# Kernel tuning notes

Measured on AMD Instinct MI355X. Metric: run time of the kernel, lower is better.

Reference implementation:

```python
import jax, jax.numpy as jnp
import numpy as np

B, S, HID = 4, 1024, 1024
NH, HD = 16, 64  # num_heads, head_size
LEFT, RIGHT = 64, 8
NUM_POS = LEFT + RIGHT + 1  # 73


def setup_inputs() -> dict:
    key = jax.random.key(0)
    ks = jax.random.split(key, 11)
    s = 0.02
    return {
        "hidden_states": jax.random.normal(ks[0], (B, S, HID), jnp.float32),
        "Wq": jax.random.normal(ks[1], (HID, HID), jnp.float32) * s,
        "bq": jax.random.normal(ks[2], (HID,), jnp.float32) * s,
        "Wk": jax.random.normal(ks[3], (HID, HID), jnp.float32) * s,
        "bk": jax.random.normal(ks[4], (HID,), jnp.float32) * s,
        "Wv": jax.random.normal(ks[5], (HID, HID), jnp.float32) * s,
        "bv": jax.random.normal(ks[6], (HID,), jnp.float32) * s,
        "Wo": jax.random.normal(ks[7], (HID, HID), jnp.float32) * s,
        "bo": jax.random.normal(ks[8], (HID,), jnp.float32) * s,
        "dist_emb": jax.random.normal(ks[9], (NUM_POS, HD), jnp.float32) * s,
    }


def reference(hidden_states, Wq, bq, Wk, bk, Wv, bv, Wo, bo, dist_emb):
    inv_sqrt_d = 1.0 / np.sqrt(HD).astype(np.float32)
    # projections; nn.Linear: x @ W.T + b
    q = (hidden_states @ Wq.T + bq).reshape(B, S, NH, HD).transpose(0, 2, 1, 3)  # bhld
    k = (hidden_states @ Wk.T + bk).reshape(B, S, NH, HD).transpose(0, 2, 1, 3)
    v = (hidden_states @ Wv.T + bv).reshape(B, S, NH, HD).transpose(0, 2, 1, 3)

    scores = jnp.einsum("bhld,bhrd->bhlr", q, k) * inv_sqrt_d

    # relative_key bias
    pos_l = jnp.arange(S)[:, None]
    pos_r = jnp.arange(S)[None, :]
    dist = jnp.clip(pos_r - pos_l, -LEFT, RIGHT) + LEFT  # [S,S] in [0, NUM_POS)
    pos_emb = dist_emb[dist]  # [S,S,HD]
    rel = jnp.einsum("bhld,lrd->bhlr", q, pos_emb) * inv_sqrt_d
    scores = scores + rel

    probs = jax.nn.softmax(scores, axis=-1)  # dropout p=0 (eval)
    ctx = jnp.einsum("bhlr,bhrd->bhld", probs, v)
    ctx = ctx.transpose(0, 2, 1, 3).reshape(B, S, HID)
    out = ctx @ Wo.T + bo
    return (out, probs)
```

## Files before the change

kernel.cpp:

```cpp
#include <hip/hip_runtime.h>


using short8 = __attribute__((ext_vector_type(8))) short;
using f32x4  = __attribute__((ext_vector_type(4))) float;
using fl4    = __attribute__((ext_vector_type(4))) float;
using u16x4  = __attribute__((ext_vector_type(4))) unsigned short;

#define MFMA16(a, b, c) __builtin_amdgcn_mfma_f32_16x16x32_bf16((a), (b), (c), 0, 0, 0)

#define SCL2E 0.18033688011112042f

__device__ __forceinline__ float bf2f(unsigned short u) {
  union { unsigned int i; float f; } c;
  c.i = ((unsigned int)u) << 16;
  return c.f;
}
__device__ __forceinline__ unsigned short f2bf(float f) {
  union { float f; unsigned int i; } c;
  c.f = f;
  unsigned int x = c.i;
  return (unsigned short)((x + 0x7fffu + ((x >> 16) & 1u)) >> 16);
}
__device__ __forceinline__ float u2f(unsigned u) {
  union { unsigned i; float f; } c;
  c.i = u;
  return c.f;
}

__device__ __forceinline__ void gload_lds16(const void* g, void* l) {
  __builtin_amdgcn_global_load_lds(
      (const __attribute__((address_space(1))) void*)g,
      (__attribute__((address_space(3))) void*)l, 16, 0, 0);
}

__global__ void cvt_f32_bf16(const float* __restrict__ in,
                             unsigned short* __restrict__ out, int n4) {
  int i = blockIdx.x * blockDim.x + threadIdx.x;
  int stride = gridDim.x * blockDim.x;
  for (; i < n4; i += stride) {
    fl4 v = ((const fl4*)in)[i];
    u16x4 o;
    o[0] = f2bf(v[0]); o[1] = f2bf(v[1]); o[2] = f2bf(v[2]); o[3] = f2bf(v[3]);
    ((u16x4*)out)[i] = o;
  }
}

__global__ void cvt_w4d(const float* __restrict__ w0, const float* __restrict__ w1,
                        const float* __restrict__ w2, const float* __restrict__ w3,
                        const float* __restrict__ de,
                        unsigned short* __restrict__ o0, unsigned short* __restrict__ o1,
                        unsigned short* __restrict__ o2, unsigned short* __restrict__ o3,
                        unsigned short* __restrict__ od) {
  if (blockIdx.x == 1024) {
    for (int i = threadIdx.x; i < 80 * 64; i += 256)
      od[i] = (i < 73 * 64) ? f2bf(de[i]) : (unsigned short)0;
    return;
  }
  const int which = blockIdx.x >> 8;
  const float* in = which == 0 ? w0 : which == 1 ? w1 : which == 2 ? w2 : w3;
  unsigned short* out = which == 0 ? o0 : which == 1 ? o1 : which == 2 ? o2 : o3;
  int i = (blockIdx.x & 255) * 256 + threadIdx.x;
#pragma unroll
  for (int it = 0; it < 4; ++it, i += 65536) {
    fl4 v = ((const fl4*)in)[i];
    u16x4 o;
    o[0] = f2bf(v[0]); o[1] = f2bf(v[1]); o[2] = f2bf(v[2]); o[3] = f2bf(v[3]);
    ((u16x4*)out)[i] = o;
  }
}

__global__ __launch_bounds__(256)
void gemm_qkv3(const unsigned short* __restrict__ X,
               const unsigned short* __restrict__ Bq,
               const unsigned short* __restrict__ Bk,
               const unsigned short* __restrict__ Bv,
               const float* __restrict__ biq, const float* __restrict__ bik,
               const float* __restrict__ biv,
               unsigned short* __restrict__ Cq, unsigned short* __restrict__ Ck,
               unsigned short* __restrict__ Cv) {
  __shared__ unsigned short lA[128 * 32];
  __shared__ unsigned short lB[128 * 32];
  const int i = blockIdx.x;
  const int wgid = (i & 7) * 96 + (i >> 3);
  const int r = wgid >> 8;
  const int id = wgid & 255;
  int bm, bn;
  const unsigned short *Aa, *Bb;
  if (r == 2) {
    bm = (id >> 5) * 128; bn = (id & 31) * 128;
    Aa = Bv; Bb = X;
  } else {
    bm = (id >> 3) * 128; bn = (id & 7) * 128;
    Aa = X; Bb = (r == 0) ? Bq : Bk;
  }
  const float* bias = (r == 0) ? biq : (r == 1) ? bik : biv;

  const int tid = threadIdx.x;
  const int wave = tid >> 6, lane = tid & 63;
  const int wm = wave >> 1, wn = wave & 1;

  f32x4 acc[4][4];
#pragma unroll
  for (int m = 0; m < 4; ++m)
#pragma unroll
    for (int n = 0; n < 4; ++n) acc[m][n] = (f32x4){0.f, 0.f, 0.f, 0.f};

  const int t0 = tid, t1 = tid + 256;
  const int ar0 = t0 >> 2, ak0 = (t0 & 3) * 8;
  const int ar1 = t1 >> 2, ak1 = (t1 & 3) * 8;
  const unsigned short* Ab = Aa + (size_t)bm * 1024;
  const unsigned short* Bbb = Bb + (size_t)bn * 1024;
  const int fr = lane & 15, fk = (lane >> 4) * 8;

  for (int kt = 0; kt < 1024; kt += 32) {
    gload_lds16(Ab + (size_t)ar0 * 1024 + kt + ak0, (void*)&lA[(wave * 64) * 8]);
    gload_lds16(Ab + (size_t)ar1 * 1024 + kt + ak1, (void*)&lA[2048 + (wave * 64) * 8]);
    gload_lds16(Bbb + (size_t)ar0 * 1024 + kt + ak0, (void*)&lB[(wave * 64) * 8]);
    gload_lds16(Bbb + (size_t)ar1 * 1024 + kt + ak1, (void*)&lB[2048 + (wave * 64) * 8]);
    __syncthreads();
    short8 af[4], bf[4];
#pragma unroll
    for (int m = 0; m < 4; ++m)
      af[m] = *(const short8*)&lA[(wm * 64 + m * 16 + fr) * 32 + fk];
#pragma unroll
    for (int n = 0; n < 4; ++n)
      bf[n] = *(const short8*)&lB[(wn * 64 + n * 16 + fr) * 32 + fk];
#pragma unroll
    for (int m = 0; m < 4; ++m)
#pragma unroll
      for (int n = 0; n < 4; ++n) acc[m][n] = MFMA16(af[m], bf[n], acc[m][n]);
    __syncthreads();
  }

  const int cr = (lane >> 4) * 4, cc = lane & 15;
#pragma unroll
  for (int m = 0; m < 4; ++m)
#pragma unroll
    for (int n = 0; n < 4; ++n) {
      const int col = bn + wn * 64 + n * 16 + cc;
#pragma unroll
      for (int g = 0; g < 4; ++g) {
        const int row = bm + wm * 64 + m * 16 + cr + g;
        if (r == 2) {
          const float v = acc[m][n][g] + bias[row];
          const int head = row >> 6, d = row & 63;
          const int b2 = col >> 10, sl = col & 1023, kk = sl & 31;
          size_t idx = ((size_t)((b2 << 4) + head) << 16) +
                       (size_t)(((sl >> 5) * 4 + (d >> 4)) * 512) +
                       (d & 15) * 32 + ((kk >> 3) * 8) + (kk & 7);
          Cv[idx] = f2bf(v);
        } else {
          const float v = acc[m][n][g] + bias[col];
          const int head = col >> 6, d = col & 63;
          const int b2 = row >> 10, sl = row & 1023;
          const int dc = d >> 3;
          const size_t hb = (size_t)((b2 << 4) + head) << 16;
          if (r == 0) {
            size_t idx = hb +
                         (size_t)((((sl >> 4) * 2 + (dc >> 2)) * 16 + (sl & 15)) * 32) +
                         (dc & 3) * 8 + (d & 7);
            Cq[idx] = f2bf(v);
          } else {
            const int kt2 = sl >> 5;
            const int p = ((sl >> 3) & 3) * 4 + (sl & 3);
            const int half = (sl >> 2) & 1;
            size_t idx = hb +
                         (size_t)((((kt2 * 2 + half) * 2 + (dc >> 2)) * 512)) +
                         p * 32 + (dc & 3) * 8 + (d & 7);
            Ck[idx] = f2bf(v);
          }
        }
      }
    }
}

__global__ __launch_bounds__(256)
void gemm_nt_f32(const unsigned short* __restrict__ A,
                 const unsigned short* __restrict__ B,
                 const float* __restrict__ bias, float* __restrict__ Cp) {
  __shared__ unsigned short lA[128 * 32];
  __shared__ unsigned short lB[128 * 32];
  const int tid = threadIdx.x;
  const int wave = tid >> 6, lane = tid & 63;
  const int wm = wave >> 1, wn = wave & 1;
  const int bm = blockIdx.x * 128, bn = blockIdx.y * 128;

  f32x4 acc[4][4];
#pragma unroll
  for (int m = 0; m < 4; ++m)
#pragma unroll
    for (int n = 0; n < 4; ++n) acc[m][n] = (f32x4){0.f, 0.f, 0.f, 0.f};

  const int t0 = tid, t1 = tid + 256;
  const int ar0 = t0 >> 2, ak0 = (t0 & 3) * 8;
  const int ar1 = t1 >> 2, ak1 = (t1 & 3) * 8;
  const unsigned short* Ab = A + (size_t)bm * 1024;
  const unsigned short* Bb = B + (size_t)bn * 1024;
  const int fr = lane & 15, fk = (lane >> 4) * 8;

  for (int kt = 0; kt < 1024; kt += 32) {
    gload_lds16(Ab + (size_t)ar0 * 1024 + kt + ak0, (void*)&lA[(wave * 64) * 8]);
    gload_lds16(Ab + (size_t)ar1 * 1024 + kt + ak1, (void*)&lA[2048 + (wave * 64) * 8]);
    gload_lds16(Bb + (size_t)ar0 * 1024 + kt + ak0, (void*)&lB[(wave * 64) * 8]);
    gload_lds16(Bb + (size_t)ar1 * 1024 + kt + ak1, (void*)&lB[2048 + (wave * 64) * 8]);
    __syncthreads();
    short8 af[4], bf[4];
#pragma unroll
    for (int m = 0; m < 4; ++m)
      af[m] = *(const short8*)&lA[(wm * 64 + m * 16 + fr) * 32 + fk];
#pragma unroll
    for (int n = 0; n < 4; ++n)
      bf[n] = *(const short8*)&lB[(wn * 64 + n * 16 + fr) * 32 + fk];
#pragma unroll
    for (int m = 0; m < 4; ++m)
#pragma unroll
      for (int n = 0; n < 4; ++n) acc[m][n] = MFMA16(af[m], bf[n], acc[m][n]);
    __syncthreads();
  }

  const int cr = (lane >> 4) * 4, cc = lane & 15;
#pragma unroll
  for (int m = 0; m < 4; ++m)
#pragma unroll
    for (int n = 0; n < 4; ++n) {
      const int col = bn + wn * 64 + n * 16 + cc;
#pragma unroll
      for (int g = 0; g < 4; ++g) {
        const int row = bm + wm * 64 + m * 16 + cr + g;
        Cp[(size_t)row * 1024 + col] = acc[m][n][g] + bias[col];
      }
    }
}

__global__ __launch_bounds__(256, 2)
void attn_kernel(const unsigned short* __restrict__ q,
                 const unsigned short* __restrict__ k,
                 const unsigned short* __restrict__ vt,
                 const unsigned short* __restrict__ demb_bf,
                 float* __restrict__ probs,
                 unsigned short* __restrict__ ctx) {
  const int i = blockIdx.x;
  const int x = i & 7, s = i >> 3;
  const int bh = ((s >> 5) << 3) + x;
  const int qseg = s & 31;
  const int hd = bh & 15, b = bh >> 4;
  const int tid = threadIdx.x, w = tid >> 6, lane = tid & 63;
  const int lq = lane & 15, Qr = lane >> 4;
  const int qA = qseg * 32, qB = qA + 16;

  __shared__ unsigned short qdc[32][78];
  __shared__ float reds[4][32];
  __shared__ float red[4][4][32][16];

  const size_t hb = (size_t)((b << 4) + hd) << 16;
  const int lo16 = lq * 32 + Qr * 8;

  const unsigned short* qh = q + hb + (size_t)(qseg * 4) * 512;
  short8 bqA0 = *(const short8*)(qh + lo16);
  short8 bqA1 = *(const short8*)(qh + 512 + lo16);
  short8 bqB0 = *(const short8*)(qh + 1024 + lo16);
  short8 bqB1 = *(const short8*)(qh + 1536 + lo16);

  for (int pgq = w; pgq < 10; pgq += 4) {
    const int qblk = pgq >= 5;
    const int pg = qblk ? pgq - 5 : pgq;
    const unsigned short* dp = demb_bf + (size_t)(pg * 16 + lq) * 64 + Qr * 8;
    short8 a0 = *(const short8*)dp;
    short8 a1 = *(const short8*)(dp + 32);
    f32x4 c = (f32x4){0.f, 0.f, 0.f, 0.f};
    c = MFMA16(a0, qblk ? bqB0 : bqA0, c);
    c = MFMA16(a1, qblk ? bqB1 : bqA1, c);
#pragma unroll
    for (int g = 0; g < 4; ++g) {
      const int p = pg * 16 + Qr * 4 + g;
      if (p < 73) qdc[qblk * 16 + lq][p] = f2bf(c[g] * SCL2E);
    }
  }
  __syncthreads();

  const float qd0A = bf2f(qdc[lq][0]),       qd72A = bf2f(qdc[lq][72]);
  const float qd0B = bf2f(qdc[16 + lq][0]),  qd72B = bf2f(qdc[16 + lq][72]);

  float ssumA = 0.f, ssumB = 0.f;
  unsigned pafA[8][4], pafB[8][4];

  const unsigned short* kh = k + hb + (size_t)(w * 8) * 2048 + lo16;
  const unsigned short* vh = vt + hb + (size_t)(w * 8) * 2048 + lo16;

#pragma unroll
  for (int t = 0; t < 8; ++t) {
    const unsigned short* kp = kh + t * 2048;
    short8 ae0 = *(const short8*)kp;
    short8 ae1 = *(const short8*)(kp + 512);
    short8 ao0 = *(const short8*)(kp + 1024);
    short8 ao1 = *(const short8*)(kp + 1536);

    f32x4 seA = (f32x4){0.f, 0.f, 0.f, 0.f}, soA = seA, seB = seA, soB = seA;
    seA = MFMA16(ae0, bqA0, seA); seA = MFMA16(ae1, bqA1, seA);
    soA = MFMA16(ao0, bqA0, soA); soA = MFMA16(ao1, bqA1, soA);
    seB = MFMA16(ae0, bqB0, seB); seB = MFMA16(ae1, bqB1, seB);
    soB = MFMA16(ao0, bqB0, soB); soB = MFMA16(ao1, bqB1, soB);

    const int tglob = w * 8 + t;
    {
      float pe[4], po[4];
      if (tglob * 32 + 31 < qA - 64) {
#pragma unroll
        for (int g = 0; g < 4; ++g) {
          pe[g] = exp2f(fmaf(seA[g], SCL2E, qd0A));
          po[g] = exp2f(fmaf(soA[g], SCL2E, qd0A));
        }
      } else if (tglob * 32 > qA + 23) {
#pragma unroll
        for (int g = 0; g < 4; ++g) {
          pe[g] = exp2f(fmaf(seA[g], SCL2E, qd72A));
          po[g] = exp2f(fmaf(soA[g], SCL2E, qd72A));
        }
      } else {
        const int c0 = tglob * 32 + Qr * 8 - (qA + lq);
#pragma unroll
        for (int g = 0; g < 4; ++g) {
          int d0 = c0 + g;     d0 = d0 < -64 ? -64 : (d0 > 8 ? 8 : d0);
          int d1 = c0 + 4 + g; d1 = d1 < -64 ? -64 : (d1 > 8 ? 8 : d1);
          pe[g] = exp2f(fmaf(seA[g], SCL2E, bf2f(qdc[lq][d0 + 64])));
          po[g] = exp2f(fmaf(soA[g], SCL2E, bf2f(qdc[lq][d1 + 64])));
        }
      }
#pragma unroll
      for (int g = 0; g < 4; ++g) ssumA += pe[g] + po[g];
      asm("v_cvt_pk_bf16_f32 %0, %1, %2" : "=v"(pafA[t][0]) : "v"(pe[0]), "v"(pe[1]));
      asm("v_cvt_pk_bf16_f32 %0, %1, %2" : "=v"(pafA[t][1]) : "v"(pe[2]), "v"(pe[3]));
      asm("v_cvt_pk_bf16_f32 %0, %1, %2" : "=v"(pafA[t][2]) : "v"(po[0]), "v"(po[1]));
      asm("v_cvt_pk_bf16_f32 %0, %1, %2" : "=v"(pafA[t][3]) : "v"(po[2]), "v"(po[3]));
    }
    {
      float pe[4], po[4];
      if (tglob * 32 + 31 < qB - 64) {
#pragma unroll
        for (int g = 0; g < 4; ++g) {
          pe[g] = exp2f(fmaf(seB[g], SCL2E, qd0B));
          po[g] = exp2f(fmaf(soB[g], SCL2E, qd0B));
        }
      } else if (tglob * 32 > qB + 23) {
#pragma unroll
        for (int g = 0; g < 4; ++g) {
          pe[g] = exp2f(fmaf(seB[g], SCL2E, qd72B));
          po[g] = exp2f(fmaf(soB[g], SCL2E, qd72B));
        }
      } else {
        const int c0 = tglob * 32 + Qr * 8 - (qB + lq);
#pragma unroll
        for (int g = 0; g < 4; ++g) {
          int d0 = c0 + g;     d0 = d0 < -64 ? -64 : (d0 > 8 ? 8 : d0);
          int d1 = c0 + 4 + g; d1 = d1 < -64 ? -64 : (d1 > 8 ? 8 : d1);
          pe[g] = exp2f(fmaf(seB[g], SCL2E, bf2f(qdc[16 + lq][d0 + 64])));
          po[g] = exp2f(fmaf(soB[g], SCL2E, bf2f(qdc[16 + lq][d1 + 64])));
        }
      }
#pragma unroll
      for (int g = 0; g < 4; ++g) ssumB += pe[g] + po[g];
      asm("v_cvt_pk_bf16_f32 %0, %1, %2" : "=v"(pafB[t][0]) : "v"(pe[0]), "v"(pe[1]));
      asm("v_cvt_pk_bf16_f32 %0, %1, %2" : "=v"(pafB[t][1]) : "v"(pe[2]), "v"(pe[3]));
      asm("v_cvt_pk_bf16_f32 %0, %1, %2" : "=v"(pafB[t][2]) : "v"(po[0]), "v"(po[1]));
      asm("v_cvt_pk_bf16_f32 %0, %1, %2" : "=v"(pafB[t][3]) : "v"(po[2]), "v"(po[3]));
    }
  }
  ssumA += __shfl_xor(ssumA, 16, 64);
  ssumA += __shfl_xor(ssumA, 32, 64);
  ssumB += __shfl_xor(ssumB, 16, 64);
  ssumB += __shfl_xor(ssumB, 32, 64);
  if (lane < 16) {
    reds[w][lane] = ssumA;
    reds[w][16 + lane] = ssumB;
  }
  __syncthreads();

  const float invA =
      1.0f / (reds[0][lq] + reds[1][lq] + reds[2][lq] + reds[3][lq]);
  const float invB = 1.0f / (reds[0][16 + lq] + reds[1][16 + lq] +
                             reds[2][16 + lq] + reds[3][16 + lq]);
  float* prowA = probs + ((size_t)bh * 1024 + qA + lq) * 1024 + w * 256 + Qr * 8;
  float* prowB = prowA + (size_t)16 * 1024;

  f32x4 oA0 = (f32x4){0.f, 0.f, 0.f, 0.f}, oA1 = oA0, oA2 = oA0, oA3 = oA0;
  f32x4 oB0 = oA0, oB1 = oA0, oB2 = oA0, oB3 = oA0;
#pragma unroll
  for (int t = 0; t < 8; ++t) {
    const unsigned short* vp = vh + t * 2048;
    short8 v0 = *(const short8*)vp;
    short8 v1 = *(const short8*)(vp + 512);
    short8 v2 = *(const short8*)(vp + 1024);
    short8 v3 = *(const short8*)(vp + 1536);

    union { unsigned u[4]; short8 s8v; } ua, ub;
    ua.u[0] = pafA[t][0]; ua.u[1] = pafA[t][1];
    ua.u[2] = pafA[t][2]; ua.u[3] = pafA[t][3];
    ub.u[0] = pafB[t][0]; ub.u[1] = pafB[t][1];
    ub.u[2] = pafB[t][2]; ub.u[3] = pafB[t][3];
    const short8 pa = ua.s8v, pb = ub.s8v;
    oA0 = MFMA16(pa, v0, oA0);
    oA1 = MFMA16(pa, v1, oA1);
    oA2 = MFMA16(pa, v2, oA2);
    oA3 = MFMA16(pa, v3, oA3);
    oB0 = MFMA16(pb, v0, oB0);
    oB1 = MFMA16(pb, v1, oB1);
    oB2 = MFMA16(pb, v2, oB2);
    oB3 = MFMA16(pb, v3, oB3);

    f32x4 p0, p1;
    p0[0] = u2f(pafA[t][0] << 16) * invA;
    p0[1] = u2f(pafA[t][0] & 0xffff0000u) * invA;
    p0[2] = u2f(pafA[t][1] << 16) * invA;
    p0[3] = u2f(pafA[t][1] & 0xffff0000u) * invA;
    p1[0] = u2f(pafA[t][2] << 16) * invA;
    p1[1] = u2f(pafA[t][2] & 0xffff0000u) * invA;
    p1[2] = u2f(pafA[t][3] << 16) * invA;
    p1[3] = u2f(pafA[t][3] & 0xffff0000u) * invA;
    *(f32x4*)&prowA[t * 32] = p0;
    *(f32x4*)&prowA[t * 32 + 4] = p1;
    f32x4 q0, q1;
    q0[0] = u2f(pafB[t][0] << 16) * invB;
    q0[1] = u2f(pafB[t][0] & 0xffff0000u) * invB;
    q0[2] = u2f(pafB[t][1] << 16) * invB;
    q0[3] = u2f(pafB[t][1] & 0xffff0000u) * invB;
    q1[0] = u2f(pafB[t][2] << 16) * invB;
    q1[1] = u2f(pafB[t][2] & 0xffff0000u) * invB;
    q1[2] = u2f(pafB[t][3] << 16) * invB;
    q1[3] = u2f(pafB[t][3] & 0xffff0000u) * invB;
    *(f32x4*)&prowB[t * 32] = q0;
    *(f32x4*)&prowB[t * 32 + 4] = q1;
  }

#pragma unroll
  for (int g = 0; g < 4; ++g) {
    red[w][0][Qr * 4 + g][lq] = oA0[g];
    red[w][1][Qr * 4 + g][lq] = oA1[g];
    red[w][2][Qr * 4 + g][lq] = oA2[g];
    red[w][3][Qr * 4 + g][lq] = oA3[g];
    red[w][0][16 + Qr * 4 + g][lq] = oB0[g];
    red[w][1][16 + Qr * 4 + g][lq] = oB1[g];
    red[w][2][16 + Qr * 4 + g][lq] = oB2[g];
    red[w][3][16 + Qr * 4 + g][lq] = oB3[g];
  }
  __syncthreads();

  {
    const int qrow = tid >> 3;
    const int d0 = (tid & 7) * 8;
    const float invq = 1.0f / (reds[0][qrow] + reds[1][qrow] +
                               reds[2][qrow] + reds[3][qrow]);
    u16x4 cv0, cv1;
#pragma unroll
    for (int j = 0; j < 8; ++j) {
      const int d = d0 + j;
      const int db = d >> 4, dd = d & 15;
      float sum = red[0][db][qrow][dd] + red[1][db][qrow][dd] +
                  red[2][db][qrow][dd] + red[3][db][qrow][dd];
      if (j < 4) cv0[j] = f2bf(sum * invq);
      else       cv1[j - 4] = f2bf(sum * invq);
    }
    unsigned short* cb =
        ctx + ((size_t)(b * 1024 + qA + qrow)) * 1024 + hd * 64 + d0;
    *(u16x4*)cb = cv0;
    *(u16x4*)(cb + 4) = cv1;
  }
}

extern "C" void kernel_launch(void* const* d_in, const int* in_sizes, int n_in,
                              void* d_out, int out_size, void* d_ws, size_t ws_size,
                              hipStream_t stream) {
  const float* hs = (const float*)d_in[0];
  const float* Wq = (const float*)d_in[1];
  const float* bq = (const float*)d_in[2];
  const float* Wk = (const float*)d_in[3];
  const float* bk = (const float*)d_in[4];
  const float* Wv = (const float*)d_in[5];
  const float* bv = (const float*)d_in[6];
  const float* Wo = (const float*)d_in[7];
  const float* bo = (const float*)d_in[8];
  const float* de = (const float*)d_in[9];

  float* out = (float*)d_out;
  float* probs = out + (size_t)4 * 1024 * 1024;

  char* ws = (char*)d_ws;
  unsigned short* Xb  = (unsigned short*)(ws);
  unsigned short* Wqb = (unsigned short*)(ws + ((size_t)8 << 20));
  unsigned short* Wkb = (unsigned short*)(ws + ((size_t)10 << 20));
  unsigned short* Wvb = (unsigned short*)(ws + ((size_t)12 << 20));
  unsigned short* Wob = (unsigned short*)(ws + ((size_t)14 << 20));
  unsigned short* Qb  = (unsigned short*)(ws + ((size_t)16 << 20));
  unsigned short* Kb  = (unsigned short*)(ws + ((size_t)24 << 20));
  unsigned short* Vt  = (unsigned short*)(ws + ((size_t)32 << 20));
  unsigned short* Db  = (unsigned short*)(ws + ((size_t)40 << 20));
  unsigned short* Cx  = Xb;

  cvt_f32_bf16<<<dim3(1024), dim3(256), 0, stream>>>(hs, Xb, (4 * 1024 * 1024) / 4);
  cvt_w4d<<<dim3(1025), dim3(256), 0, stream>>>(Wq, Wk, Wv, Wo, de,
                                                Wqb, Wkb, Wvb, Wob, Db);

  gemm_qkv3<<<dim3(768), dim3(256), 0, stream>>>(Xb, Wqb, Wkb, Wvb, bq, bk, bv,
                                                 Qb, Kb, Vt);

  attn_kernel<<<dim3(2048), dim3(256), 0, stream>>>(Qb, Kb, Vt, Db, probs, Cx);

  gemm_nt_f32<<<dim3(32, 8), dim3(256), 0, stream>>>(Cx, Wob, bo, out);
}
```

Measured before the change: 173.6 us.

## Process two 32-query tiles per attention block, overlapping second QK with first PV

New measurement: 200.4 us. +15.4%, slower.

```diff
diff --git a/kernel.cpp b/kernel.cpp
--- a/kernel.cpp
+++ b/kernel.cpp
@@ -241,52 +241,110 @@
                  unsigned short* __restrict__ ctx) {
   const int i = blockIdx.x;
   const int x = i & 7, s = i >> 3;
-  const int bh = ((s >> 5) << 3) + x;
-  const int qseg = s & 31;
+  const int bh = ((s >> 4) << 3) + x;
+  const int j = s & 15;
   const int hd = bh & 15, b = bh >> 4;
   const int tid = threadIdx.x, w = tid >> 6, lane = tid & 63;
   const int lq = lane & 15, Qr = lane >> 4;
-  const int qA = qseg * 32, qB = qA + 16;
-
-  __shared__ unsigned short qdc[32][78];
-  __shared__ float reds[4][32];
+  const int qA1 = j * 64, qB1 = qA1 + 16, qA2 = qA1 + 32, qB2 = qA1 + 48;
+
+  __shared__ unsigned short qdc[2][32][78];
+  __shared__ float reds[2][4][32];
   __shared__ float red[4][4][32][16];
 
   const size_t hb = (size_t)((b << 4) + hd) << 16;
   const int lo16 = lq * 32 + Qr * 8;
 
-  const unsigned short* qh = q + hb + (size_t)(qseg * 4) * 512;
-  short8 bqA0 = *(const short8*)(qh + lo16);
-  short8 bqA1 = *(const short8*)(qh + 512 + lo16);
-  short8 bqB0 = *(const short8*)(qh + 1024 + lo16);
-  short8 bqB1 = *(const short8*)(qh + 1536 + lo16);
-
-  for (int pgq = w; pgq < 10; pgq += 4) {
-    const int qblk = pgq >= 5;
-    const int pg = qblk ? pgq - 5 : pgq;
+  const unsigned short* qh1 = q + hb + (size_t)(j * 8) * 512;
+  const unsigned short* qh2 = qh1 + 2048;
+  short8 q1A0 = *(const short8*)(qh1 + lo16);
+  short8 q1A1 = *(const short8*)(qh1 + 512 + lo16);
+  short8 q1B0 = *(const short8*)(qh1 + 1024 + lo16);
+  short8 q1B1 = *(const short8*)(qh1 + 1536 + lo16);
+  short8 q2A0 = *(const short8*)(qh2 + lo16);
+  short8 q2A1 = *(const short8*)(qh2 + 512 + lo16);
+  short8 q2B0 = *(const short8*)(qh2 + 1024 + lo16);
+  short8 q2B1 = *(const short8*)(qh2 + 1536 + lo16);
+
+  for (int pgq = w; pgq < 20; pgq += 4) {
+    const int u = pgq >= 10;
+    const int pp = pgq - u * 10;
+    const int qblk = pp >= 5;
+    const int pg = pp - qblk * 5;
     const unsigned short* dp = demb_bf + (size_t)(pg * 16 + lq) * 64 + Qr * 8;
     short8 a0 = *(const short8*)dp;
     short8 a1 = *(const short8*)(dp + 32);
+    short8 f0 = u ? (qblk ? q2B0 : q2A0) : (qblk ? q1B0 : q1A0);
+    short8 f1 = u ? (qblk ? q2B1 : q2A1) : (qblk ? q1B1 : q1A1);
     f32x4 c = (f32x4){0.f, 0.f, 0.f, 0.f};
-    c = MFMA16(a0, qblk ? bqB0 : bqA0, c);
-    c = MFMA16(a1, qblk ? bqB1 : bqA1, c);
+    c = MFMA16(a0, f0, c);
+    c = MFMA16(a1, f1, c);
 #pragma unroll
     for (int g = 0; g < 4; ++g) {
       const int p = pg * 16 + Qr * 4 + g;
-      if (p < 73) qdc[qblk * 16 + lq][p] = f2bf(c[g] * SCL2E);
+      if (p < 73) qdc[u][qblk * 16 + lq][p] = f2bf(c[g] * SCL2E);
     }
   }
   __syncthreads();
 
-  const float qd0A = bf2f(qdc[lq][0]),       qd72A = bf2f(qdc[lq][72]);
-  const float qd0B = bf2f(qdc[16 + lq][0]),  qd72B = bf2f(qdc[16 + lq][72]);
-
-  float ssumA = 0.f, ssumB = 0.f;
-  unsigned pafA[8][4], pafB[8][4];
+  const float qd0A1 = bf2f(qdc[0][lq][0]),      qd72A1 = bf2f(qdc[0][lq][72]);
+  const float qd0B1 = bf2f(qdc[0][16 + lq][0]), qd72B1 = bf2f(qdc[0][16 + lq][72]);
+  const float qd0A2 = bf2f(qdc[1][lq][0]),      qd72A2 = bf2f(qdc[1][lq][72]);
+  const float qd0B2 = bf2f(qdc[1][16 + lq][0]), qd72B2 = bf2f(qdc[1][16 + lq][72]);
 
   const unsigned short* kh = k + hb + (size_t)(w * 8) * 2048 + lo16;
   const unsigned short* vh = vt + hb + (size_t)(w * 8) * 2048 + lo16;
 
+#define QKEXP(se, so, qAx, qd0x, qd72x, UU, LQOFF, paf, ssum, tglob)          \
+  {                                                                           \
+    float pe[4], po[4];                                                       \
+    if ((tglob)*32 + 31 < (qAx)-64) {                                         \
+      _Pragma("unroll") for (int g = 0; g < 4; ++g) {                         \
+        pe[g] = exp2f(fmaf(se[g], SCL2E, qd0x));                              \
+        po[g] = exp2f(fmaf(so[g], SCL2E, qd0x));                              \
+      }                                                                       \
+    } else if ((tglob)*32 > (qAx) + 23) {                                     \
+      _Pragma("unroll") for (int g = 0; g < 4; ++g) {                         \
+        pe[g] = exp2f(fmaf(se[g], SCL2E, qd72x));                             \
+        po[g] = exp2f(fmaf(so[g], SCL2E, qd72x));                             \
+      }                                                                       \
+    } else {                                                                  \
+      const int c0 = (tglob)*32 + Qr * 8 - ((qAx) + lq);                      \
+      _Pragma("unroll") for (int g = 0; g < 4; ++g) {                         \
+        int d0 = c0 + g;     d0 = d0 < -64 ? -64 : (d0 > 8 ? 8 : d0);         \
+        int d1 = c0 + 4 + g; d1 = d1 < -64 ? -64 : (d1 > 8 ? 8 : d1);         \
+        pe[g] = exp2f(fmaf(se[g], SCL2E, bf2f(qdc[UU][(LQOFF) + lq][d0 + 64])));\
+        po[g] = exp2f(fmaf(so[g], SCL2E, bf2f(qdc[UU][(LQOFF) + lq][d1 + 64])));\
+      }                                                                       \
+    }                                                                         \
+    _Pragma("unroll") for (int g = 0; g < 4; ++g) ssum += pe[g] + po[g];      \
+    asm("v_cvt_pk_bf16_f32 %0, %1, %2" : "=v"(paf[0]) : "v"(pe[0]), "v"(pe[1]));\
+    asm("v_cvt_pk_bf16_f32 %0, %1, %2" : "=v"(paf[1]) : "v"(pe[2]), "v"(pe[3]));\
+    asm("v_cvt_pk_bf16_f32 %0, %1, %2" : "=v"(paf[2]) : "v"(po[0]), "v"(po[1]));\
+    asm("v_cvt_pk_bf16_f32 %0, %1, %2" : "=v"(paf[3]) : "v"(po[2]), "v"(po[3]));\
+  }
+
+#define STORE8(paf, inv, prow, t)                                             \
+  {                                                                           \
+    f32x4 p0, p1;                                                             \
+    p0[0] = u2f(paf[0] << 16) * inv;                                          \
+    p0[1] = u2f(paf[0] & 0xffff0000u) * inv;                                  \
+    p0[2] = u2f(paf[1] << 16) * inv;                                          \
+    p0[3] = u2f(paf[1] & 0xffff0000u) * inv;                                  \
+    p1[0] = u2f(paf[2] << 16) * inv;                                          \
+    p1[1] = u2f(paf[2] & 0xffff0000u) * inv;                                  \
+    p1[2] = u2f(paf[3] << 16) * inv;                                          \
+    p1[3] = u2f(paf[3] & 0xffff0000u) * inv;                                  \
+    *(f32x4*)&prow[(t)*32] = p0;                                              \
+    *(f32x4*)&prow[(t)*32 + 4] = p1;                                          \
+  }
+
+#define PACK8(paf) ({ union { unsigned uu4[4]; short8 s8v; } _u;              \
+    _u.uu4[0] = paf[0]; _u.uu4[1] = paf[1];                                   \
+    _u.uu4[2] = paf[2]; _u.uu4[3] = paf[3]; _u.s8v; })
+
+  float sA1 = 0.f, sB1 = 0.f;
+  unsigned paf1A[8][4], paf1B[8][4];
 #pragma unroll
   for (int t = 0; t < 8; ++t) {
     const unsigned short* kp = kh + t * 2048;
@@ -294,96 +352,31 @@
     short8 ae1 = *(const short8*)(kp + 512);
     short8 ao0 = *(const short8*)(kp + 1024);
     short8 ao1 = *(const short8*)(kp + 1536);
-
-    f32x4 seA = (f32x4){0.f, 0.f, 0.f, 0.f}, soA = seA, seB = seA, soB = seA;
-    seA = MFMA16(ae0, bqA0, seA); seA = MFMA16(ae1, bqA1, seA);
-    soA = MFMA16(ao0, bqA0, soA); soA = MFMA16(ao1, bqA1, soA);
-    seB = MFMA16(ae0, bqB0, seB); seB = MFMA16(ae1, bqB1, seB);
-    soB = MFMA16(ao0, bqB0, soB); soB = MFMA16(ao1, bqB1, soB);
-
-    const int tglob = w * 8 + t;
-    {
-      float pe[4], po[4];
-      if (tglob * 32 + 31 < qA - 64) {
-#pragma unroll
-        for (int g = 0; g < 4; ++g) {
-          pe[g] = exp2f(fmaf(seA[g], SCL2E, qd0A));
-          po[g] = exp2f(fmaf(soA[g], SCL2E, qd0A));
-        }
-      } else if (tglob * 32 > qA + 23) {
-#pragma unroll
-        for (int g = 0; g < 4; ++g) {
-          pe[g] = exp2f(fmaf(seA[g], SCL2E, qd72A));
-          po[g] = exp2f(fmaf(soA[g], SCL2E, qd72A));
-        }
-      } else {
-        const int c0 = tglob * 32 + Qr * 8 - (qA + lq);
-#pragma unroll
-        for (int g = 0; g < 4; ++g) {
-          int d0 = c0 + g;     d0 = d0 < -64 ? -64 : (d0 > 8 ? 8 : d0);
-          int d1 = c0 + 4 + g; d1 = d1 < -64 ? -64 : (d1 > 8 ? 8 : d1);
-          pe[g] = exp2f(fmaf(seA[g], SCL2E, bf2f(qdc[lq][d0 + 64])));
-          po[g] = exp2f(fmaf(soA[g], SCL2E, bf2f(qdc[lq][d1 + 64])));
-        }
-      }
-#pragma unroll
-      for (int g = 0; g < 4; ++g) ssumA += pe[g] + po[g];
-      asm("v_cvt_pk_bf16_f32 %0, %1, %2" : "=v"(pafA[t][0]) : "v"(pe[0]), "v"(pe[1]));
-      asm("v_cvt_pk_bf16_f32 %0, %1, %2" : "=v"(pafA[t][1]) : "v"(pe[2]), "v"(pe[3]));
-      asm("v_cvt_pk_bf16_f32 %0, %1, %2" : "=v"(pafA[t][2]) : "v"(po[0]), "v"(po[1]));
-      asm("v_cvt_pk_bf16_f32 %0, %1, %2" : "=v"(pafA[t][3]) : "v"(po[2]), "v"(po[3]));
-    }
-    {
-      float pe[4], po[4];
-      if (tglob * 32 + 31 < qB - 64) {
-#pragma unroll
-        for (int g = 0; g < 4; ++g) {
-          pe[g] = exp2f(fmaf(seB[g], SCL2E, qd0B));
-          po[g] = exp2f(fmaf(soB[g], SCL2E, qd0B));
-        }
-      } else if (tglob * 32 > qB + 23) {
-#pragma unroll
-        for (int g = 0; g < 4; ++g) {
-          pe[g] = exp2f(fmaf(seB[g], SCL2E, qd72B));
-          po[g] = exp2f(fmaf(soB[g], SCL2E, qd72B));
-        }
-      } else {
-        const int c0 = tglob * 32 + Qr * 8 - (qB + lq);
-#pragma unroll
-        for (int g = 0; g < 4; ++g) {
-          int d0 = c0 + g;     d0 = d0 < -64 ? -64 : (d0 > 8 ? 8 : d0);
-          int d1 = c0 + 4 + g; d1 = d1 < -64 ? -64 : (d1 > 8 ? 8 : d1);
-          pe[g] = exp2f(fmaf(seB[g], SCL2E, bf2f(qdc[16 + lq][d0 + 64])));
-          po[g] = exp2f(fmaf(soB[g], SCL2E, bf2f(qdc[16 + lq][d1 + 64])));
-        }
-      }
-#pragma unroll
-      for (int g = 0; g < 4; ++g) ssumB += pe[g] + po[g];
-      asm("v_cvt_pk_bf16_f32 %0, %1, %2" : "=v"(pafB[t][0]) : "v"(pe[0]), "v"(pe[1]));
-      asm("v_cvt_pk_bf16_f32 %0, %1, %2" : "=v"(pafB[t][1]) : "v"(pe[2]), "v"(pe[3]));
-      asm("v_cvt_pk_bf16_f32 %0, %1, %2" : "=v"(pafB[t][2]) : "v"(po[0]), "v"(po[1]));
-      asm("v_cvt_pk_bf16_f32 %0, %1, %2" : "=v"(pafB[t][3]) : "v"(po[2]), "v"(po[3]));
-    }
-  }
-  ssumA += __shfl_xor(ssumA, 16, 64);
-  ssumA += __shfl_xor(ssumA, 32, 64);
-  ssumB += __shfl_xor(ssumB, 16, 64);
-  ssumB += __shfl_xor(ssumB, 32, 64);
-  if (lane < 16) {
-    reds[w][lane] = ssumA;
-    reds[w][16 + lane] = ssumB;
-  }
+    f32x4 se = (f32x4){0.f, 0.f, 0.f, 0.f}, so = se, se2 = se, so2 = se;
+    se = MFMA16(ae0, q1A0, se);  se = MFMA16(ae1, q1A1, se);
+    so = MFMA16(ao0, q1A0, so);  so = MFMA16(ao1, q1A1, so);
+    se2 = MFMA16(ae0, q1B0, se2); se2 = MFMA16(ae1, q1B1, se2);
+    so2 = MFMA16(ao0, q1B0, so2); so2 = MFMA16(ao1, q1B1, so2);
+    const int tg = w * 8 + t;
+    QKEXP(se, so, qA1, qd0A1, qd72A1, 0, 0, paf1A[t], sA1, tg);
+    QKEXP(se2, so2, qB1, qd0B1, qd72B1, 0, 16, paf1B[t], sB1, tg);
+  }
+  sA1 += __shfl_xor(sA1, 16, 64); sA1 += __shfl_xor(sA1, 32, 64);
+  sB1 += __shfl_xor(sB1, 16, 64); sB1 += __shfl_xor(sB1, 32, 64);
+  if (lane < 16) { reds[0][w][lane] = sA1; reds[0][w][16 + lane] = sB1; }
   __syncthreads();
 
-  const float invA =
-      1.0f / (reds[0][lq] + reds[1][lq] + reds[2][lq] + reds[3][lq]);
-  const float invB = 1.0f / (reds[0][16 + lq] + reds[1][16 + lq] +
-                             reds[2][16 + lq] + reds[3][16 + lq]);
-  float* prowA = probs + ((size_t)bh * 1024 + qA + lq) * 1024 + w * 256 + Qr * 8;
-  float* prowB = prowA + (size_t)16 * 1024;
-
-  f32x4 oA0 = (f32x4){0.f, 0.f, 0.f, 0.f}, oA1 = oA0, oA2 = oA0, oA3 = oA0;
-  f32x4 oB0 = oA0, oB1 = oA0, oB2 = oA0, oB3 = oA0;
+  const float invA1 = 1.0f / (reds[0][0][lq] + reds[0][1][lq] +
+                              reds[0][2][lq] + reds[0][3][lq]);
+  const float invB1 = 1.0f / (reds[0][0][16 + lq] + reds[0][1][16 + lq] +
+                              reds[0][2][16 + lq] + reds[0][3][16 + lq]);
+  float* prowA1 = probs + ((size_t)bh * 1024 + qA1 + lq) * 1024 + w * 256 + Qr * 8;
+  float* prowB1 = prowA1 + (size_t)16 * 1024;
+
+  float sA2 = 0.f, sB2 = 0.f;
+  unsigned paf2A[8][4], paf2B[8][4];
+  f32x4 o1A0 = (f32x4){0.f, 0.f, 0.f, 0.f}, o1A1 = o1A0, o1A2 = o1A0, o1A3 = o1A0;
+  f32x4 o1B0 = o1A0, o1B1 = o1A0, o1B2 = o1A0, o1B3 = o1A0;
 #pragma unroll
   for (int t = 0; t < 8; ++t) {
     const unsigned short* vp = vh + t * 2048;
@@ -391,79 +384,128 @@
     short8 v1 = *(const short8*)(vp + 512);
     short8 v2 = *(const short8*)(vp + 1024);
     short8 v3 = *(const short8*)(vp + 1536);
-
-    union { unsigned u[4]; short8 s8v; } ua, ub;
-    ua.u[0] = pafA[t][0]; ua.u[1] = pafA[t][1];
-    ua.u[2] = pafA[t][2]; ua.u[3] = pafA[t][3];
-    ub.u[0] = pafB[t][0]; ub.u[1] = pafB[t][1];
-    ub.u[2] = pafB[t][2]; ub.u[3] = pafB[t][3];
-    const short8 pa = ua.s8v, pb = ub.s8v;
-    oA0 = MFMA16(pa, v0, oA0);
-    oA1 = MFMA16(pa, v1, oA1);
-    oA2 = MFMA16(pa, v2, oA2);
-    oA3 = MFMA16(pa, v3, oA3);
-    oB0 = MFMA16(pb, v0, oB0);
-    oB1 = MFMA16(pb, v1, oB1);
-    oB2 = MFMA16(pb, v2, oB2);
-    oB3 = MFMA16(pb, v3, oB3);
-
-    f32x4 p0, p1;
-    p0[0] = u2f(pafA[t][0] << 16) * invA;
-    p0[1] = u2f(pafA[t][0] & 0xffff0000u) * invA;
-    p0[2] = u2f(pafA[t][1] << 16) * invA;
-    p0[3] = u2f(pafA[t][1] & 0xffff0000u) * invA;
-    p1[0] = u2f(pafA[t][2] << 16) * invA;
-    p1[1] = u2f(pafA[t][2] & 0xffff0000u) * invA;
-    p1[2] = u2f(pafA[t][3] << 16) * invA;
-    p1[3] = u2f(pafA[t][3] & 0xffff0000u) * invA;
-    *(f32x4*)&prowA[t * 32] = p0;
-    *(f32x4*)&prowA[t * 32 + 4] = p1;
-    f32x4 q0, q1;
-    q0[0] = u2f(pafB[t][0] << 16) * invB;
-    q0[1] = u2f(pafB[t][0] & 0xffff0000u) * invB;
-    q0[2] = u2f(pafB[t][1] << 16) * invB;
-    q0[3] = u2f(pafB[t][1] & 0xffff0000u) * invB;
-    q1[0] = u2f(pafB[t][2] << 16) * invB;
-    q1[1] = u2f(pafB[t][2] & 0xffff0000u) * invB;
-    q1[2] = u2f(pafB[t][3] << 16) * invB;
-    q1[3] = u2f(pafB[t][3] & 0xffff0000u) * invB;
-    *(f32x4*)&prowB[t * 32] = q0;
-    *(f32x4*)&prowB[t * 32 + 4] = q1;
-  }
-
+    const unsigned short* kp = kh + t * 2048;
+    short8 ae0 = *(const short8*)kp;
+    short8 ae1 = *(const short8*)(kp + 512);
+    short8 ao0 = *(const short8*)(kp + 1024);
+    short8 ao1 = *(const short8*)(kp + 1536);
+
+    const short8 pa = PACK8(paf1A[t]);
+    const short8 pb = PACK8(paf1B[t]);
+    o1A0 = MFMA16(pa, v0, o1A0); o1A1 = MFMA16(pa, v1, o1A1);
+    o1A2 = MFMA16(pa, v2, o1A2); o1A3 = MFMA16(pa, v3, o1A3);
+    o1B0 = MFMA16(pb, v0, o1B0); o1B1 = MFMA16(pb, v1, o1B1);
+    o1B2 = MFMA16(pb, v2, o1B2); o1B3 = MFMA16(pb, v3, o1B3);
+    STORE8(paf1A[t], invA1, prowA1, t);
+    STORE8(paf1B[t], invB1, prowB1, t);
+    f32x4 se = (f32x4){0.f, 0.f, 0.f, 0.f}, so = se, se2 = se, so2 = se;
+    se = MFMA16(ae0, q2A0, se);  se = MFMA16(ae1, q2A1, se);
+    so = MFMA16(ao0, q2A0, so);  so = MFMA16(ao1, q2A1, so);
+    se2 = MFMA16(ae0, q2B0, se2); se2 = MFMA16(ae1, q2B1, se2);
+    so2 = MFMA16(ao0, q2B0, so2); so2 = MFMA16(ao1, q2B1, so2);
+    const int tg = w * 8 + t;
+    QKEXP(se, so, qA2, qd0A2, qd72A2, 1, 0, paf2A[t], sA2, tg);
+    QKEXP(se2, so2, qB2, qd0B2, qd72B2, 1, 16, paf2B[t], sB2, tg);
+  }
+  sA2 += __shfl_xor(sA2, 16, 64); sA2 += __shfl_xor(sA2, 32, 64);
+  sB2 += __shfl_xor(sB2, 16, 64); sB2 += __shfl_xor(sB2, 32, 64);
+  if (lane < 16) { reds[1][w][lane] = sA2; reds[1][w][16 + lane] = sB2; }
 #pragma unroll
   for (int g = 0; g < 4; ++g) {
-    red[w][0][Qr * 4 + g][lq] = oA0[g];
-    red[w][1][Qr * 4 + g][lq] = oA1[g];
-    red[w][2][Qr * 4 + g][lq] = oA2[g];
-    red[w][3][Qr * 4 + g][lq] = oA3[g];
-    red[w][0][16 + Qr * 4 + g][lq] = oB0[g];
-    red[w][1][16 + Qr * 4 + g][lq] = oB1[g];
-    red[w][2][16 + Qr * 4 + g][lq] = oB2[g];
-    red[w][3][16 + Qr * 4 + g][lq] = oB3[g];
+    red[w][0][Qr * 4 + g][lq] = o1A0[g];
+    red[w][1][Qr * 4 + g][lq] = o1A1[g];
+    red[w][2][Qr * 4 + g][lq] = o1A2[g];
+    red[w][3][Qr * 4 + g][lq] = o1A3[g];
+    red[w][0][16 + Qr * 4 + g][lq] = o1B0[g];
+    red[w][1][16 + Qr * 4 + g][lq] = o1B1[g];
+    red[w][2][16 + Qr * 4 + g][lq] = o1B2[g];
+    red[w][3][16 + Qr * 4 + g][lq] = o1B3[g];
   }
   __syncthreads();
 
   {
     const int qrow = tid >> 3;
     const int d0 = (tid & 7) * 8;
-    const float invq = 1.0f / (reds[0][qrow] + reds[1][qrow] +
-                               reds[2][qrow] + reds[3][qrow]);
+    const float invq = 1.0f / (reds[0][0][qrow] + reds[0][1][qrow] +
+                               reds[0][2][qrow] + reds[0][3][qrow]);
     u16x4 cv0, cv1;
 #pragma unroll
-    for (int j = 0; j < 8; ++j) {
-      const int d = d0 + j;
+    for (int jj = 0; jj < 8; ++jj) {
+      const int d = d0 + jj;
       const int db = d >> 4, dd = d & 15;
       float sum = red[0][db][qrow][dd] + red[1][db][qrow][dd] +
                   red[2][db][qrow][dd] + red[3][db][qrow][dd];
-      if (j < 4) cv0[j] = f2bf(sum * invq);
-      else       cv1[j - 4] = f2bf(sum * invq);
+      if (jj < 4) cv0[jj] = f2bf(sum * invq);
+      else        cv1[jj - 4] = f2bf(sum * invq);
     }
     unsigned short* cb =
-        ctx + ((size_t)(b * 1024 + qA + qrow)) * 1024 + hd * 64 + d0;
+        ctx + ((size_t)(b * 1024 + qA1 + qrow)) * 1024 + hd * 64 + d0;
     *(u16x4*)cb = cv0;
     *(u16x4*)(cb + 4) = cv1;
   }
+  __syncthreads();
+
+  const float invA2 = 1.0f / (reds[1][0][lq] + reds[1][1][lq] +
+                              reds[1][2][lq] + reds[1][3][lq]);
+  const float invB2 = 1.0f / (reds[1][0][16 + lq] + reds[1][1][16 + lq] +
+                              reds[1][2][16 + lq] + reds[1][3][16 + lq]);
+  float* prowA2 = probs + ((size_t)bh * 1024 + qA2 + lq) * 1024 + w * 256 + Qr * 8;
+  float* prowB2 = prowA2 + (size_t)16 * 1024;
+
+  f32x4 o2A0 = (f32x4){0.f, 0.f, 0.f, 0.f}, o2A1 = o2A0, o2A2 = o2A0, o2A3 = o2A0;
+  f32x4 o2B0 = o2A0, o2B1 = o2A0, o2B2 = o2A0, o2B3 = o2A0;
+#pragma unroll
+  for (int t = 0; t < 8; ++t) {
+    const unsigned short* vp = vh + t * 2048;
+    short8 v0 = *(const short8*)vp;
+    short8 v1 = *(const short8*)(vp + 512);
+    short8 v2 = *(const short8*)(vp + 1024);
+    short8 v3 = *(const short8*)(vp + 1536);
+    const short8 pa = PACK8(paf2A[t]);
+    const short8 pb = PACK8(paf2B[t]);
+    o2A0 = MFMA16(pa, v0, o2A0); o2A1 = MFMA16(pa, v1, o2A1);
+    o2A2 = MFMA16(pa, v2, o2A2); o2A3 = MFMA16(pa, v3, o2A3);
+    o2B0 = MFMA16(pb, v0, o2B0); o2B1 = MFMA16(pb, v1, o2B1);
+    o2B2 = MFMA16(pb, v2, o2B2); o2B3 = MFMA16(pb, v3, o2B3);
+    STORE8(paf2A[t], invA2, prowA2, t);
+    STORE8(paf2B[t], invB2, prowB2, t);
+  }
+#pragma unroll
+  for (int g = 0; g < 4; ++g) {
+    red[w][0][Qr * 4 + g][lq] = o2A0[g];
+    red[w][1][Qr * 4 + g][lq] = o2A1[g];
+    red[w][2][Qr * 4 + g][lq] = o2A2[g];
+    red[w][3][Qr * 4 + g][lq] = o2A3[g];
+    red[w][0][16 + Qr * 4 + g][lq] = o2B0[g];
+    red[w][1][16 + Qr * 4 + g][lq] = o2B1[g];
+    red[w][2][16 + Qr * 4 + g][lq] = o2B2[g];
+    red[w][3][16 + Qr * 4 + g][lq] = o2B3[g];
+  }
+  __syncthreads();
+
+  {
+    const int qrow = tid >> 3;
+    const int d0 = (tid & 7) * 8;
+    const float invq = 1.0f / (reds[1][0][qrow] + reds[1][1][qrow] +
+                               reds[1][2][qrow] + reds[1][3][qrow]);
+    u16x4 cv0, cv1;
+#pragma unroll
+    for (int jj = 0; jj < 8; ++jj) {
+      const int d = d0 + jj;
+      const int db = d >> 4, dd = d & 15;
+      float sum = red[0][db][qrow][dd] + red[1][db][qrow][dd] +
+                  red[2][db][qrow][dd] + red[3][db][qrow][dd];
+      if (jj < 4) cv0[jj] = f2bf(sum * invq);
+      else        cv1[jj - 4] = f2bf(sum * invq);
+    }
+    unsigned short* cb =
+        ctx + ((size_t)(b * 1024 + qA2 + qrow)) * 1024 + hd * 64 + d0;
+    *(u16x4*)cb = cv0;
+    *(u16x4*)(cb + 4) = cv1;
+  }
+#undef QKEXP
+#undef STORE8
+#undef PACK8
 }
 
 extern "C" void kernel_launch(void* const* d_in, const int* in_sizes, int n_in,
@@ -502,7 +544,7 @@
   gemm_qkv3<<<dim3(768), dim3(256), 0, stream>>>(Xb, Wqb, Wkb, Wvb, bq, bk, bv,
                                                  Qb, Kb, Vt);
 
-  attn_kernel<<<dim3(2048), dim3(256), 0, stream>>>(Qb, Kb, Vt, Db, probs, Cx);
+  attn_kernel<<<dim3(1024), dim3(256), 0, stream>>>(Qb, Kb, Vt, Db, probs, Cx);
 
   gemm_nt_f32<<<dim3(32, 8), dim3(256), 0, stream>>>(Cx, Wob, bo, out);
 }
```
